# Kernel tuning notes

Measured on AMD Instinct MI355X. Metric: run time of the kernel, lower is better.

Reference implementation:

```python
import jax, jax.numpy as jnp
import numpy as np
from jax import lax

R = 8
SCALE = 1.0          # alpha / r with alpha == r
RESCALE = 1.0        # rescale_factor computed at init (constant)
PAD, DIL, GROUPS, K = 1, 1, 1, 3
BS, CIN, COUT, L = 128, 64, 64, 8192
EMB, HID = 256, 256
BN_EPS = 1e-5


def _mlp(x, w1, b1, g, beta, w2, b2):
    # Linear -> BatchNorm1d(eval, running mean=0, var=1) -> GELU(exact) -> Linear
    h = x @ w1.T + b1
    h = h * (g / np.float32(np.sqrt(1.0 + BN_EPS))) + beta
    h = jax.nn.gelu(h, approximate=False)
    return h @ w2.T + b2


def _conv1d(x, w, groups):
    # x: [N, C, L], w: [O, C/groups, K]
    return lax.conv_general_dilated(
        x, w, window_strides=(1,), padding=[(PAD, PAD)], rhs_dilation=(DIL,),
        dimension_numbers=("NCH", "OIH", "NCH"), feature_group_count=groups)


def setup_inputs() -> dict:
    key = jax.random.key(0)
    ks = jax.random.split(key, 20)
    n = lambda i, shape, s=1.0: (jax.random.normal(ks[i], shape, dtype=jnp.float32) * s)
    return {
        "X": n(0, (BS, CIN, L)),
        "a_embedding": n(1, (BS, EMB)),
        "b_embedding": n(2, (BS, EMB)),
        "A_w1": n(3, (HID, EMB), 0.06), "A_b1": n(4, (HID,), 0.02),
        "A_bn_g": 1.0 + n(5, (HID,), 0.05), "A_bn_b": n(6, (HID,), 0.02),
        "A_w2": n(7, (CIN * R // GROUPS, HID), 0.06), "A_b2": n(8, (CIN * R // GROUPS,), 0.02),
        "B_w1": n(9, (HID, EMB), 0.06), "B_b1": n(10, (HID,), 0.02),
        "B_bn_g": 1.0 + n(11, (HID,), 0.05), "B_bn_b": n(12, (HID,), 0.02),
        "B_w2": n(13, (COUT * R * K, HID), 0.06), "B_b2": n(14, (COUT * R * K,), 0.02),
        "base_w": n(15, (COUT, CIN // GROUPS, K), 0.08), "base_b": n(16, (COUT,), 0.02),
    }


def reference(X, a_embedding, b_embedding,
              A_w1, A_b1, A_bn_g, A_bn_b, A_w2, A_b2,
              B_w1, B_b1, B_bn_g, B_bn_b, B_w2, B_b2,
              base_w, base_b):
    bs = X.shape[0]
    # rescale applied under no_grad in the original -> inputs carry no grad
    a = lax.stop_gradient(a_embedding * RESCALE)
    b = lax.stop_gradient(b_embedding * RESCALE)
    # per-sample low-rank factors
    A = _mlp(a, A_w1, A_b1, A_bn_g, A_bn_b, A_w2, A_b2).reshape(bs, CIN // GROUPS, R)
    B = _mlp(b, B_w1, B_b1, B_bn_g, B_bn_b, B_w2, B_b2).reshape(bs, R, COUT * K)
    # dynamic conv weight: bmm(A, B) -> [bs, Cin/g, Cout, K] -> [bs, Cout, Cin/g, K]
    W = jnp.einsum("bir,brm->bim", A, B).reshape(bs, CIN // GROUPS, COUT, K)
    W = jnp.transpose(W, (0, 2, 1, 3))  # [bs, Cout, Cin/g, K]
    # per-sample conv (equivalent to F.conv1d with groups=bs*groups trick)
    lora = jax.vmap(lambda x, w: _conv1d(x[None], w, GROUPS)[0])(X, W)  # [bs, Cout, L]
    base = _conv1d(X, base_w, GROUPS) + base_b[None, :, None]
    return lora * SCALE + base
```

## Files before the change

### kernel.cpp

```cpp
#include <hip/hip_runtime.h>
#include <hip/hip_bf16.h>

#define BS    128
#define NCIN  64
#define NCOUT 64
#define LLEN  8192
#define NK    3
#define NR    8
#define NEMB  256
#define NHID  256
#define WPS   (NCOUT * NCIN * NK)
#define NT    512

typedef __attribute__((ext_vector_type(4)))  float  f32x4;
typedef __attribute__((ext_vector_type(16))) float  f32x16;
typedef __attribute__((ext_vector_type(8)))  __bf16 bf16x8;

__device__ float  g_A[BS * 512];
__device__ float  g_B[BS * 1536];
__device__ __bf16 g_Wb[BS * WPS];

__global__ __launch_bounds__(256) void mlp_kernel(
    const float* __restrict__ a_emb, const float* __restrict__ b_emb,
    const float* __restrict__ A_w1, const float* __restrict__ A_b1,
    const float* __restrict__ A_g,  const float* __restrict__ A_beta,
    const float* __restrict__ A_w2, const float* __restrict__ A_b2,
    const float* __restrict__ B_w1, const float* __restrict__ B_b1,
    const float* __restrict__ B_g,  const float* __restrict__ B_beta,
    const float* __restrict__ B_w2, const float* __restrict__ B_b2)
{
    __shared__ __align__(16) float emb_s[NEMB];
    __shared__ __align__(16) float h_s[NHID];

    const int t      = threadIdx.x;
    const int branch = blockIdx.x >> 7;
    const int b      = blockIdx.x & 127;

    const float* emb  = (branch ? b_emb : a_emb) + (size_t)b * NEMB;
    const float* w1   = branch ? B_w1 : A_w1;
    const float* b1   = branch ? B_b1 : A_b1;
    const float* gg   = branch ? B_g  : A_g;
    const float* bt   = branch ? B_beta : A_beta;
    const float* w2   = branch ? B_w2 : A_w2;
    const float* b2   = branch ? B_b2 : A_b2;
    float* outp       = (branch ? g_B : g_A) + (size_t)b * (branch ? 1536 : 512);
    const int nloops  = branch ? 6 : 2;

    emb_s[t] = emb[t];
    __syncthreads();

    {
        float acc = b1[t];
        const f32x4* wr = (const f32x4*)(w1 + (size_t)t * NEMB);
        const f32x4* es = (const f32x4*)emb_s;
        for (int e = 0; e < NEMB / 4; ++e) {
            f32x4 w = wr[e], a = es[e];
            acc += w[0]*a[0] + w[1]*a[1] + w[2]*a[2] + w[3]*a[3];
        }
        float h = acc * (gg[t] * (1.0f / sqrtf(1.0f + 1e-5f))) + bt[t];
        h = 0.5f * h * (1.0f + erff(h * 0.70710678118654752f));
        h_s[t] = h;
    }
    __syncthreads();

    for (int oo = 0; oo < nloops; ++oo) {
        const int o = oo * 256 + t;
        float acc = b2[o];
        const f32x4* wr = (const f32x4*)(w2 + (size_t)o * NHID);
        const f32x4* hs = (const f32x4*)h_s;
        for (int e = 0; e < NHID / 4; ++e) {
            f32x4 w = wr[e], h = hs[e];
            acc += w[0]*h[0] + w[1]*h[1] + w[2]*h[2] + w[3]*h[3];
        }
        outp[o] = acc;
    }
}

__global__ __launch_bounds__(256) void assemble_kernel(const float* __restrict__ base_w)
{
    const int b  = blockIdx.x >> 2;
    const int q  = blockIdx.x & 3;
    const int t  = threadIdx.x;
    const int ci = t & 63;

    float Ar[NR];
    const f32x4* Ap = (const f32x4*)(g_A + (size_t)b * 512 + ci * NR);
    f32x4 a0 = Ap[0], a1 = Ap[1];
    Ar[0]=a0[0]; Ar[1]=a0[1]; Ar[2]=a0[2]; Ar[3]=a0[3];
    Ar[4]=a1[0]; Ar[5]=a1[1]; Ar[6]=a1[2]; Ar[7]=a1[3];

    const float* Bp = g_B + (size_t)b * 1536;
    for (int i = 0; i < 12; ++i) {
        const int w  = q * 3072 + i * 256 + t;
        const int k  = w >> 12;
        const int co = (w >> 6) & 63;
        float v = base_w[(size_t)(co * 64 + ci) * 3 + k];
        #pragma unroll
        for (int r = 0; r < NR; ++r) v += Ar[r] * Bp[r * 192 + co * 3 + k];
        g_Wb[(size_t)b * WPS + w] = (__bf16)v;
    }
}

__global__ __launch_bounds__(256, 2) void conv_kernel(
    const float* __restrict__ X, const float* __restrict__ base_b,
    float* __restrict__ out)
{
    __shared__ __align__(16) __bf16 xt[(NT + 2) * 64];

    const int swz  = (blockIdx.x & 7) * 256 + (blockIdx.x >> 3);
    const int b    = swz >> 4;
    const int tile = swz & 15;
    const int l0   = tile * NT;

    const int t     = threadIdx.x;
    const int lane  = t & 63;
    const int wave  = t >> 6;
    const int l31   = lane & 31;
    const int khalf = lane >> 5;
    const int wco   = wave >> 1;
    const int wl    = wave & 1;
    const int lb    = t & 63;
    const int ch    = t >> 6;

    const float* xbase = X + (size_t)b * NCIN * LLEN;

    #pragma unroll
    for (int pass = 0; pass < 2; ++pass) {
        const int och = ch + pass * 4;
        f32x4 v[8][2];
        const float* xb = xbase + l0 + lb * 8;
        #pragma unroll
        for (int c = 0; c < 8; ++c) {
            const float* xr = xb + (size_t)(och * 8 + c) * LLEN;
            v[c][0] = *(const f32x4*)(xr);
            v[c][1] = *(const f32x4*)(xr + 4);
        }
        #pragma unroll
        for (int j = 0; j < 8; ++j) {
            const int lp = lb * 8 + j + 1;
            bf16x8 w;
            #pragma unroll
            for (int c = 0; c < 8; ++c) w[c] = (__bf16)v[c][j >> 2][j & 3];
            const int blk = och ^ (lp & 7) ^ ((lp >> 3) & 7);
            *(bf16x8*)(xt + lp * 64 + blk * 8) = w;
        }
    }
    if (t < 128) {
        const int ci    = t & 63;
        const int right = t >> 6;
        const int gl    = right ? (l0 + NT) : (l0 - 1);
        const int lp    = right ? (NT + 1) : 0;
        const float hv  = (gl >= 0 && gl < LLEN) ? xbase[(size_t)ci * LLEN + gl] : 0.0f;
        const int blk   = (ci >> 3) ^ (lp & 7) ^ ((lp >> 3) & 7);
        xt[lp * 64 + blk * 8 + (ci & 7)] = (__bf16)hv;
    }
    __syncthreads();

    bf16x8 af[3][4];
    {
        const __bf16* wb = g_Wb + (size_t)b * WPS + (wco * 32 + l31) * 64 + khalf * 8;
        #pragma unroll
        for (int tap = 0; tap < 3; ++tap)
            #pragma unroll
            for (int c16 = 0; c16 < 4; ++c16)
                af[tap][c16] = *(const bf16x8*)(wb + tap * 4096 + c16 * 16);
    }

    f32x16 acc[8] = {};
    #pragma unroll
    for (int tap = 0; tap < 3; ++tap)
        #pragma unroll
        for (int c16 = 0; c16 < 4; ++c16)
            #pragma unroll
            for (int n = 0; n < 8; ++n) {
                const int R   = wl * 256 + n * 32 + l31 + tap;
                const int blk = (c16 * 2 + khalf) ^ (R & 7) ^ ((R >> 3) & 7);
                bf16x8 bfr = *(const bf16x8*)(xt + R * 64 + blk * 8);
                acc[n] = __builtin_amdgcn_mfma_f32_32x32x16_bf16(af[tap][c16], bfr, acc[n], 0, 0, 0);
            }

    #pragma unroll
    for (int reg = 0; reg < 16; ++reg) {
        const int col = (reg & 3) + 8 * (reg >> 2) + 4 * khalf;
        const int co  = wco * 32 + col;
        const float bb = base_b[co];
        float* op = out + (size_t)(b * NCOUT + co) * LLEN + l0 + wl * 256 + l31;
        #pragma unroll
        for (int n = 0; n < 8; ++n)
            op[n * 32] = acc[n][reg] + bb;
    }
}

extern "C" void kernel_launch(void* const* d_in, const int* in_sizes, int n_in,
                              void* d_out, int out_size, void* d_ws, size_t ws_size,
                              hipStream_t stream)
{
    const float* X      = (const float*)d_in[0];
    const float* a_emb  = (const float*)d_in[1];
    const float* b_emb  = (const float*)d_in[2];
    const float* A_w1   = (const float*)d_in[3];
    const float* A_b1   = (const float*)d_in[4];
    const float* A_g    = (const float*)d_in[5];
    const float* A_beta = (const float*)d_in[6];
    const float* A_w2   = (const float*)d_in[7];
    const float* A_b2   = (const float*)d_in[8];
    const float* B_w1   = (const float*)d_in[9];
    const float* B_b1   = (const float*)d_in[10];
    const float* B_g    = (const float*)d_in[11];
    const float* B_beta = (const float*)d_in[12];
    const float* B_w2   = (const float*)d_in[13];
    const float* B_b2   = (const float*)d_in[14];
    const float* base_w = (const float*)d_in[15];
    const float* base_b = (const float*)d_in[16];

    float* out = (float*)d_out;

    mlp_kernel<<<2 * BS, 256, 0, stream>>>(a_emb, b_emb,
        A_w1, A_b1, A_g, A_beta, A_w2, A_b2,
        B_w1, B_b1, B_g, B_beta, B_w2, B_b2);

    assemble_kernel<<<4 * BS, 256, 0, stream>>>(base_w);

    conv_kernel<<<2048, 256, 0, stream>>>(X, base_b, out);
}
```

Before: 188.7 us.

## Process two L-halves per conv block, prefetching second half into registers

Each conv block now covers 1024 positions instead of 512, and the grid drops to 1024 blocks. All X loads for both halves are issued up front, and the second half is parked in registers as packed bf16 while the first half is computed. The second half is then written into the reused LDS tile. This is meant to overlap global loads with MFMA work and amortise the per-block weight-fragment load. The extra held registers (64 VGPRs of bf16) risk lowering occupancy or causing spills under launch_bounds(256,2), and the smaller grid reduces parallelism.

```diff
diff --git a/kernel.cpp b/kernel.cpp
--- a/kernel.cpp
+++ b/kernel.cpp
@@ -10,7 +10,8 @@
 #define NEMB  256
 #define NHID  256
 #define WPS   (NCOUT * NCIN * NK)
-#define NT    512
+#define NH    512
+#define NT    1024
 
 typedef __attribute__((ext_vector_type(4)))  float  f32x4;
 typedef __attribute__((ext_vector_type(16))) float  f32x16;
@@ -105,12 +106,11 @@
     const float* __restrict__ X, const float* __restrict__ base_b,
     float* __restrict__ out)
 {
-    __shared__ __align__(16) __bf16 xt[(NT + 2) * 64];
-
-    const int swz  = (blockIdx.x & 7) * 256 + (blockIdx.x >> 3);
-    const int b    = swz >> 4;
-    const int tile = swz & 15;
-    const int l0   = tile * NT;
+    __shared__ __align__(16) __bf16 xt[(NH + 2) * 64];
+
+    const int swz = (blockIdx.x & 7) * 128 + (blockIdx.x >> 3);
+    const int b   = swz >> 3;
+    const int l0  = (swz & 7) * NT;
 
     const int t     = threadIdx.x;
     const int lane  = t & 63;
@@ -124,71 +124,111 @@
 
     const float* xbase = X + (size_t)b * NCIN * LLEN;
 
+    bf16x8 af[3][4];
+    {
+        const __bf16* wb = g_Wb + (size_t)b * WPS + (wco * 32 + l31) * 64 + khalf * 8;
+        #pragma unroll
+        for (int tap = 0; tap < 3; ++tap)
+            #pragma unroll
+            for (int c16 = 0; c16 < 4; ++c16)
+                af[tap][c16] = *(const bf16x8*)(wb + tap * 4096 + c16 * 16);
+    }
+
+    const int hci = t & 63;
+    const int hrt = (t >> 6) & 1;
+    float hv1 = 0.0f, hv2 = 0.0f;
+    if (t < 128) {
+        const int gl1 = hrt ? (l0 + NH) : (l0 - 1);
+        if (gl1 >= 0 && gl1 < LLEN) hv1 = xbase[(size_t)hci * LLEN + gl1];
+        const int gl2 = hrt ? (l0 + 2 * NH) : (l0 + NH - 1);
+        if (gl2 >= 0 && gl2 < LLEN) hv2 = xbase[(size_t)hci * LLEN + gl2];
+    }
+
+    bf16x8 s[2][8];
     #pragma unroll
     for (int pass = 0; pass < 2; ++pass) {
         const int och = ch + pass * 4;
-        f32x4 v[8][2];
-        const float* xb = xbase + l0 + lb * 8;
+        const float* xr0 = xbase + (size_t)(och * 8) * LLEN + l0 + lb * 8;
+        f32x4 v1[8][2], v2[8][2];
         #pragma unroll
         for (int c = 0; c < 8; ++c) {
-            const float* xr = xb + (size_t)(och * 8 + c) * LLEN;
-            v[c][0] = *(const f32x4*)(xr);
-            v[c][1] = *(const f32x4*)(xr + 4);
+            const float* xr = xr0 + (size_t)c * LLEN;
+            v1[c][0] = *(const f32x4*)(xr);
+            v1[c][1] = *(const f32x4*)(xr + 4);
+        }
+        #pragma unroll
+        for (int c = 0; c < 8; ++c) {
+            const float* xr = xr0 + (size_t)c * LLEN + NH;
+            v2[c][0] = *(const f32x4*)(xr);
+            v2[c][1] = *(const f32x4*)(xr + 4);
         }
         #pragma unroll
         for (int j = 0; j < 8; ++j) {
-            const int lp = lb * 8 + j + 1;
-            bf16x8 w;
-            #pragma unroll
-            for (int c = 0; c < 8; ++c) w[c] = (__bf16)v[c][j >> 2][j & 3];
+            const int lp  = lb * 8 + j + 1;
             const int blk = och ^ (lp & 7) ^ ((lp >> 3) & 7);
-            *(bf16x8*)(xt + lp * 64 + blk * 8) = w;
+            bf16x8 w1, w2;
+            #pragma unroll
+            for (int c = 0; c < 8; ++c) {
+                w1[c] = (__bf16)v1[c][j >> 2][j & 3];
+                w2[c] = (__bf16)v2[c][j >> 2][j & 3];
+            }
+            *(bf16x8*)(xt + lp * 64 + blk * 8) = w1;
+            s[pass][j] = w2;
         }
     }
     if (t < 128) {
-        const int ci    = t & 63;
-        const int right = t >> 6;
-        const int gl    = right ? (l0 + NT) : (l0 - 1);
-        const int lp    = right ? (NT + 1) : 0;
-        const float hv  = (gl >= 0 && gl < LLEN) ? xbase[(size_t)ci * LLEN + gl] : 0.0f;
-        const int blk   = (ci >> 3) ^ (lp & 7) ^ ((lp >> 3) & 7);
-        xt[lp * 64 + blk * 8 + (ci & 7)] = (__bf16)hv;
-    }
-    __syncthreads();
-
-    bf16x8 af[3][4];
-    {
-        const __bf16* wb = g_Wb + (size_t)b * WPS + (wco * 32 + l31) * 64 + khalf * 8;
+        const int lp  = hrt ? (NH + 1) : 0;
+        const int blk = (hci >> 3) ^ (lp & 7) ^ ((lp >> 3) & 7);
+        xt[lp * 64 + blk * 8 + (hci & 7)] = (__bf16)hv1;
+    }
+    __syncthreads();
+
+    auto compute_half = [&](int loff) {
+        f32x16 acc[8] = {};
         #pragma unroll
         for (int tap = 0; tap < 3; ++tap)
             #pragma unroll
             for (int c16 = 0; c16 < 4; ++c16)
-                af[tap][c16] = *(const bf16x8*)(wb + tap * 4096 + c16 * 16);
-    }
-
-    f32x16 acc[8] = {};
+                #pragma unroll
+                for (int n = 0; n < 8; ++n) {
+                    const int R   = wl * 256 + n * 32 + l31 + tap;
+                    const int blk = (c16 * 2 + khalf) ^ (R & 7) ^ ((R >> 3) & 7);
+                    bf16x8 bfr = *(const bf16x8*)(xt + R * 64 + blk * 8);
+                    acc[n] = __builtin_amdgcn_mfma_f32_32x32x16_bf16(af[tap][c16], bfr, acc[n], 0, 0, 0);
+                }
+        #pragma unroll
+        for (int reg = 0; reg < 16; ++reg) {
+            const int col = (reg & 3) + 8 * (reg >> 2) + 4 * khalf;
+            const int co  = wco * 32 + col;
+            const float bb = base_b[co];
+            float* op = out + (size_t)(b * NCOUT + co) * LLEN + l0 + loff + wl * 256 + l31;
+            #pragma unroll
+            for (int n = 0; n < 8; ++n)
+                op[n * 32] = acc[n][reg] + bb;
+        }
+    };
+
+    compute_half(0);
+    __syncthreads();
+
     #pragma unroll
-    for (int tap = 0; tap < 3; ++tap)
-        #pragma unroll
-        for (int c16 = 0; c16 < 4; ++c16)
-            #pragma unroll
-            for (int n = 0; n < 8; ++n) {
-                const int R   = wl * 256 + n * 32 + l31 + tap;
-                const int blk = (c16 * 2 + khalf) ^ (R & 7) ^ ((R >> 3) & 7);
-                bf16x8 bfr = *(const bf16x8*)(xt + R * 64 + blk * 8);
-                acc[n] = __builtin_amdgcn_mfma_f32_32x32x16_bf16(af[tap][c16], bfr, acc[n], 0, 0, 0);
-            }
-
-    #pragma unroll
-    for (int reg = 0; reg < 16; ++reg) {
-        const int col = (reg & 3) + 8 * (reg >> 2) + 4 * khalf;
-        const int co  = wco * 32 + col;
-        const float bb = base_b[co];
-        float* op = out + (size_t)(b * NCOUT + co) * LLEN + l0 + wl * 256 + l31;
-        #pragma unroll
-        for (int n = 0; n < 8; ++n)
-            op[n * 32] = acc[n][reg] + bb;
-    }
+    for (int pass = 0; pass < 2; ++pass) {
+        const int och = ch + pass * 4;
+        #pragma unroll
+        for (int j = 0; j < 8; ++j) {
+            const int lp  = lb * 8 + j + 1;
+            const int blk = och ^ (lp & 7) ^ ((lp >> 3) & 7);
+            *(bf16x8*)(xt + lp * 64 + blk * 8) = s[pass][j];
+        }
+    }
+    if (t < 128) {
+        const int lp  = hrt ? (NH + 1) : 0;
+        const int blk = (hci >> 3) ^ (lp & 7) ^ ((lp >> 3) & 7);
+        xt[lp * 64 + blk * 8 + (hci & 7)] = (__bf16)hv2;
+    }
+    __syncthreads();
+
+    compute_half(NH);
 }
 
 extern "C" void kernel_launch(void* const* d_in, const int* in_sizes, int n_in,
@@ -221,5 +261,5 @@
 
     assemble_kernel<<<4 * BS, 256, 0, stream>>>(base_w);
 
-    conv_kernel<<<2048, 256, 0, stream>>>(X, base_b, out);
-}
+    conv_kernel<<<1024, 256, 0, stream>>>(X, base_b, out);
+}
```

Measured after the change: 253.3 us. 1.34x slower.

## Split MLP into batched hidden and output kernels with register-blocked weight reuse

Applied to the files above, without the earlier changes.

Replaces the per-sample MLP kernel with two kernels. Each thread now handles one sample and a block of 32 output features, using wave-uniform weight rows and a transposed hidden buffer in global memory. Every weight row is read once per block and shared across all 128 samples, instead of each of 256 blocks re-reading the full weight matrices. The cost is an extra kernel launch, an intermediate round-trip through global memory, and far fewer blocks (8 and 32), so only a fraction of the GPU is occupied.

```diff
diff --git a/kernel.cpp b/kernel.cpp
--- a/kernel.cpp
+++ b/kernel.cpp
@@ -16,63 +16,91 @@
 typedef __attribute__((ext_vector_type(16))) float  f32x16;
 typedef __attribute__((ext_vector_type(8)))  __bf16 bf16x8;
 
+__device__ float  g_h[2][NHID * BS];
 __device__ float  g_A[BS * 512];
 __device__ float  g_B[BS * 1536];
 __device__ __bf16 g_Wb[BS * WPS];
 
-__global__ __launch_bounds__(256) void mlp_kernel(
+__global__ __launch_bounds__(256) void mlp_hid(
     const float* __restrict__ a_emb, const float* __restrict__ b_emb,
     const float* __restrict__ A_w1, const float* __restrict__ A_b1,
     const float* __restrict__ A_g,  const float* __restrict__ A_beta,
+    const float* __restrict__ B_w1, const float* __restrict__ B_b1,
+    const float* __restrict__ B_g,  const float* __restrict__ B_beta)
+{
+    const int t      = threadIdx.x;
+    const int branch = blockIdx.x >> 2;
+    const int och    = blockIdx.x & 3;
+    const int s      = (t & 63) + (t >> 7) * 64;
+    const int og     = __builtin_amdgcn_readfirstlane((t >> 6) & 1);
+    const int o0     = och * 64 + og * 32;
+
+    const float* emb = (branch ? b_emb : a_emb) + (size_t)s * NEMB;
+    const float* w1  = (branch ? B_w1 : A_w1) + (size_t)o0 * NEMB;
+    const float* b1  = (branch ? B_b1 : A_b1) + o0;
+    const float* gg  = (branch ? B_g  : A_g)  + o0;
+    const float* bt  = (branch ? B_beta : A_beta) + o0;
+    float* hout = g_h[branch];
+
+    float acc[32];
+    #pragma unroll
+    for (int i = 0; i < 32; ++i) acc[i] = b1[i];
+
+    for (int e = 0; e < NEMB / 4; ++e) {
+        f32x4 em = *(const f32x4*)(emb + e * 4);
+        #pragma unroll
+        for (int i = 0; i < 32; ++i) {
+            f32x4 w = *(const f32x4*)(w1 + (size_t)i * NEMB + e * 4);
+            acc[i] += w[0]*em[0] + w[1]*em[1] + w[2]*em[2] + w[3]*em[3];
+        }
+    }
+    const float bnc = 1.0f / sqrtf(1.0f + 1e-5f);
+    #pragma unroll
+    for (int i = 0; i < 32; ++i) {
+        float h = acc[i] * (gg[i] * bnc) + bt[i];
+        h = 0.5f * h * (1.0f + erff(h * 0.70710678118654752f));
+        hout[(size_t)(o0 + i) * BS + s] = h;
+    }
+}
+
+__global__ __launch_bounds__(256) void mlp_out(
     const float* __restrict__ A_w2, const float* __restrict__ A_b2,
-    const float* __restrict__ B_w1, const float* __restrict__ B_b1,
-    const float* __restrict__ B_g,  const float* __restrict__ B_beta,
     const float* __restrict__ B_w2, const float* __restrict__ B_b2)
 {
-    __shared__ __align__(16) float emb_s[NEMB];
-    __shared__ __align__(16) float h_s[NHID];
-
-    const int t      = threadIdx.x;
-    const int branch = blockIdx.x >> 7;
-    const int b      = blockIdx.x & 127;
-
-    const float* emb  = (branch ? b_emb : a_emb) + (size_t)b * NEMB;
-    const float* w1   = branch ? B_w1 : A_w1;
-    const float* b1   = branch ? B_b1 : A_b1;
-    const float* gg   = branch ? B_g  : A_g;
-    const float* bt   = branch ? B_beta : A_beta;
-    const float* w2   = branch ? B_w2 : A_w2;
-    const float* b2   = branch ? B_b2 : A_b2;
-    float* outp       = (branch ? g_B : g_A) + (size_t)b * (branch ? 1536 : 512);
-    const int nloops  = branch ? 6 : 2;
-
-    emb_s[t] = emb[t];
-    __syncthreads();
-
-    {
-        float acc = b1[t];
-        const f32x4* wr = (const f32x4*)(w1 + (size_t)t * NEMB);
-        const f32x4* es = (const f32x4*)emb_s;
-        for (int e = 0; e < NEMB / 4; ++e) {
-            f32x4 w = wr[e], a = es[e];
-            acc += w[0]*a[0] + w[1]*a[1] + w[2]*a[2] + w[3]*a[3];
-        }
-        float h = acc * (gg[t] * (1.0f / sqrtf(1.0f + 1e-5f))) + bt[t];
-        h = 0.5f * h * (1.0f + erff(h * 0.70710678118654752f));
-        h_s[t] = h;
-    }
-    __syncthreads();
-
-    for (int oo = 0; oo < nloops; ++oo) {
-        const int o = oo * 256 + t;
-        float acc = b2[o];
-        const f32x4* wr = (const f32x4*)(w2 + (size_t)o * NHID);
-        const f32x4* hs = (const f32x4*)h_s;
-        for (int e = 0; e < NHID / 4; ++e) {
-            f32x4 w = wr[e], h = hs[e];
-            acc += w[0]*h[0] + w[1]*h[1] + w[2]*h[2] + w[3]*h[3];
-        }
-        outp[o] = acc;
+    const int blk    = blockIdx.x;
+    const int branch = (blk >= 8) ? 1 : 0;
+    const int chunk  = branch ? (blk - 8) : blk;
+    const int t   = threadIdx.x;
+    const int s   = (t & 63) + (t >> 7) * 64;
+    const int og  = __builtin_amdgcn_readfirstlane((t >> 6) & 1);
+    const int o0  = chunk * 64 + og * 32;
+
+    const float* w2 = (branch ? B_w2 : A_w2) + (size_t)o0 * NHID;
+    const float* b2 = (branch ? B_b2 : A_b2) + o0;
+    const float* h  = g_h[branch];
+    float* outp = branch ? g_B : g_A;
+    const int ostr = branch ? 1536 : 512;
+
+    float acc[32];
+    #pragma unroll
+    for (int i = 0; i < 32; ++i) acc[i] = b2[i];
+
+    for (int e = 0; e < NHID / 4; ++e) {
+        const float h0 = h[(size_t)(e * 4 + 0) * BS + s];
+        const float h1 = h[(size_t)(e * 4 + 1) * BS + s];
+        const float h2 = h[(size_t)(e * 4 + 2) * BS + s];
+        const float h3 = h[(size_t)(e * 4 + 3) * BS + s];
+        #pragma unroll
+        for (int i = 0; i < 32; ++i) {
+            f32x4 w = *(const f32x4*)(w2 + (size_t)i * NHID + e * 4);
+            acc[i] += w[0]*h0 + w[1]*h1 + w[2]*h2 + w[3]*h3;
+        }
+    }
+    float* op = outp + (size_t)s * ostr + o0;
+    #pragma unroll
+    for (int i = 0; i < 32; i += 4) {
+        f32x4 v = { acc[i], acc[i+1], acc[i+2], acc[i+3] };
+        *(f32x4*)(op + i) = v;
     }
 }
 
@@ -215,9 +243,10 @@
 
     float* out = (float*)d_out;
 
-    mlp_kernel<<<2 * BS, 256, 0, stream>>>(a_emb, b_emb,
-        A_w1, A_b1, A_g, A_beta, A_w2, A_b2,
-        B_w1, B_b1, B_g, B_beta, B_w2, B_b2);
+    mlp_hid<<<8, 256, 0, stream>>>(a_emb, b_emb,
+        A_w1, A_b1, A_g, A_beta, B_w1, B_b1, B_g, B_beta);
+
+    mlp_out<<<32, 256, 0, stream>>>(A_w2, A_b2, B_w2, B_b2);
 
     assemble_kernel<<<4 * BS, 256, 0, stream>>>(base_w);
 
```

Result: slower. 303.8 us (+61.1%).
